# Optimization experiments

Hardware: AMD Instinct MI355X
Metric: run time of the kernel (lower is better)

## Reference

```python
import jax, jax.numpy as jnp
import numpy as np

N_NODES = 50000
HEADS = 8
NEG_SLOPE = 0.2


def _gat_conv(x, src, dst, n, W, a_src, a_dst, b, concat):
    # W: [H*C, F_in], a_src/a_dst: [H, C], b: [H*C] or [C]
    H, C = a_src.shape
    h = (x @ W.T).reshape(-1, H, C)                      # [N, H, C]
    al_src = jnp.einsum('nhc,hc->nh', h, a_src)          # [N, H]
    al_dst = jnp.einsum('nhc,hc->nh', h, a_dst)          # [N, H]
    e = jax.nn.leaky_relu(al_src[src] + al_dst[dst], NEG_SLOPE)  # [E, H]
    # segment softmax over incoming edges of each dst node
    m = jax.lax.stop_gradient(jax.ops.segment_max(e, dst, num_segments=n))
    ee = jnp.exp(e - m[dst])
    denom = jax.ops.segment_sum(ee, dst, num_segments=n)
    alpha = ee / denom[dst]                              # [E, H]
    out = jax.ops.segment_sum(alpha[:, :, None] * h[src], dst, num_segments=n)  # [N, H, C]
    out = out.reshape(n, H * C) if concat else out.mean(axis=1)
    return out + b


def setup_inputs() -> dict:
    key = jax.random.key(0)
    ks = jax.random.split(key, 12)
    N, F_in, Hd, H, Ncls = N_NODES, 128, 32, HEADS, 40
    E = 800000
    x = jax.random.normal(ks[0], (N, F_in), dtype=jnp.float32)
    edge_index = jax.random.randint(ks[1], (2, E), 0, N, dtype=jnp.int64)
    s1 = 1.0 / np.sqrt(F_in)
    W1 = jax.random.normal(ks[2], (H * Hd, F_in), dtype=jnp.float32) * s1
    a_src1 = jax.random.normal(ks[3], (H, Hd), dtype=jnp.float32) * 0.1
    a_dst1 = jax.random.normal(ks[4], (H, Hd), dtype=jnp.float32) * 0.1
    b1 = jnp.zeros((H * Hd,), dtype=jnp.float32)
    s2 = 1.0 / np.sqrt(H * Hd)
    W2 = jax.random.normal(ks[5], (H * Ncls, H * Hd), dtype=jnp.float32) * s2
    a_src2 = jax.random.normal(ks[6], (H, Ncls), dtype=jnp.float32) * 0.1
    a_dst2 = jax.random.normal(ks[7], (H, Ncls), dtype=jnp.float32) * 0.1
    b2 = jnp.zeros((Ncls,), dtype=jnp.float32)
    return {"x": x, "edge_index": edge_index,
            "W1": W1, "a_src1": a_src1, "a_dst1": a_dst1, "b1": b1,
            "W2": W2, "a_src2": a_src2, "a_dst2": a_dst2, "b2": b2}


def reference(x, edge_index, W1, a_src1, a_dst1, b1, W2, a_src2, a_dst2, b2):
    n = x.shape[0]
    # PyG GATConv default: add self loops
    loop = jnp.arange(n, dtype=edge_index.dtype)
    src = jnp.concatenate([edge_index[0], loop])
    dst = jnp.concatenate([edge_index[1], loop])
    # layer 1 (concat heads) -> ELU; dropout identity in eval mode
    h = _gat_conv(x, src, dst, n, W1, a_src1, a_dst1, b1, concat=True)
    h = jax.nn.elu(h)
    # layer 2 (mean over heads)
    out = _gat_conv(h, src, dst, n, W2, a_src2, a_dst2, b2, concat=False)
    return jax.nn.log_softmax(out, axis=1)
```

## Files before the change

kernel.cpp:

```cpp
#include <hip/hip_runtime.h>
#include <hip/hip_bf16.h>
#include <math.h>

typedef unsigned short ushort_t;
typedef unsigned char uchar_t;
typedef __attribute__((ext_vector_type(8))) short short8;
typedef __attribute__((ext_vector_type(4))) float f32x4;
typedef __attribute__((ext_vector_type(2))) float f32x2;
typedef __attribute__((ext_vector_type(4))) unsigned short u16x4;

#define LOG2E 1.44269504088896f

static __device__ __forceinline__ float b2f(ushort_t u) {
    union { unsigned int i; float f; } v; v.i = ((unsigned int)u) << 16; return v.f;
}
static __device__ __forceinline__ ushort_t f2b(float f) {
    unsigned int x = __float_as_uint(f);
    unsigned int r = (x + 0x7fffu + ((x >> 16) & 1u)) >> 16;
    return (ushort_t)r;
}
static __device__ __forceinline__ uchar_t f2e4m3(float f) {
    int r = __builtin_amdgcn_cvt_pk_fp8_f32(f, f, 0, false);
    return (uchar_t)(r & 0xff);
}
static __device__ __forceinline__ float exp2fast(float x) {
    return __builtin_amdgcn_exp2f(x);
}


template<int K, int Cd>
static __device__ void wa_item(const float* __restrict__ W, const float* __restrict__ as,
                               const float* __restrict__ ad, ushort_t* __restrict__ Bext,
                               int rowoff, int tid) {
    int col = tid / K, k = tid - col * K;
    const float* a = (col < 8) ? as : ad;
    int h = col & 7;
    float s = 0.f;
    #pragma unroll 4
    for (int c = 0; c < Cd; ++c)
        s += W[(size_t)(h * Cd + c) * K + k] * a[h * Cd + c];
    Bext[(size_t)(rowoff + col) * K + k] = f2b(s * LOG2E);
}

__global__ void prep_kernel(const float* __restrict__ W1, const float* __restrict__ W2,
                            const float* __restrict__ as1, const float* __restrict__ ad1,
                            const float* __restrict__ as2, const float* __restrict__ ad2,
                            ushort_t* __restrict__ w1b, ushort_t* __restrict__ w2b,
                            float* als1, float* als2, uchar_t* h1f8, uchar_t* h2f8, int n) {
    int b = blockIdx.x, t = threadIdx.x;
    if (b < 40) {
        for (int i = b * 256 + t; i < 8192 + 20480; i += 40 * 256) {
            if (i < 8192) {
                float4 v = *(const float4*)(W1 + i * 4);
                u16x4 o = { f2b(v.x), f2b(v.y), f2b(v.z), f2b(v.w) };
                *(u16x4*)(w1b + i * 4) = o;
            } else {
                int j = i - 8192;
                float4 v = *(const float4*)(W2 + j * 4);
                u16x4 o = { f2b(v.x), f2b(v.y), f2b(v.z), f2b(v.w) };
                *(u16x4*)(w2b + j * 4) = o;
            }
        }
    } else if (b < 64) {
        for (int i = (b - 40) * 256 + t; i < 2048 + 4096; i += 24 * 256) {
            if (i < 2048) wa_item<128, 32>(W1, as1, ad1, w1b, 256, i);
            else          wa_item<256, 40>(W2, as2, ad2, w2b, 320, i - 2048);
        }
    } else {
        if (t < 8) { als1[(size_t)n * 8 + t] = -1e30f; als2[(size_t)n * 8 + t] = -1e30f; }
        h1f8[(size_t)n * 256 + t] = 0;
        h2f8[(size_t)n * 320 + t] = 0;
        if (t < 64) h2f8[(size_t)n * 320 + 256 + t] = 0;
    }
}


__global__ void convx_count_kernel(const float* __restrict__ x, ushort_t* __restrict__ xb, int n4x,
                                   const int* __restrict__ ei, int E, int n, int* __restrict__ deg) {
    int b = blockIdx.x, t = threadIdx.x;
    if (b < 2048) {
        for (int i = b * 256 + t; i < n4x; i += 2048 * 256) {
            float4 v = *(const float4*)(x + i * 4);
            u16x4 o = { f2b(v.x), f2b(v.y), f2b(v.z), f2b(v.w) };
            *(u16x4*)(xb + i * 4) = o;
        }
    } else {
        int e = (b - 2048) * 256 + t;
        int Etot = E + n;
        if (e < Etot) {
            int dst = (e < E) ? ei[E + e] : (e - E);
            atomicAdd(&deg[dst], 1);
        }
    }
}


__global__ void scan_part_kernel(const int* __restrict__ deg, int* __restrict__ bsum, int n) {
    int i = blockIdx.x * 256 + threadIdx.x;
    int v = (i < n) ? ((deg[i] + 7) & ~7) : 0;
    #pragma unroll
    for (int off = 1; off < 64; off <<= 1) v += __shfl_xor(v, off);
    __shared__ int ws[4];
    int wid = threadIdx.x >> 6, lane = threadIdx.x & 63;
    if (lane == 0) ws[wid] = v;
    __syncthreads();
    if (threadIdx.x == 0) bsum[blockIdx.x] = ws[0] + ws[1] + ws[2] + ws[3];
}

__global__ void scan_top_kernel(int* __restrict__ bsum, int nb) {
    int t = threadIdx.x;
    int v = (t < nb) ? bsum[t] : 0;
    int val = v;
    int lane = t & 63, wid = t >> 6;
    #pragma unroll
    for (int off = 1; off < 64; off <<= 1) {
        int nv = __shfl_up(val, off);
        if (lane >= off) val += nv;
    }
    __shared__ int ws[4];
    if (lane == 63) ws[wid] = val;
    __syncthreads();
    int pre = 0;
    for (int w = 0; w < 4; ++w) if (w < wid) pre += ws[w];
    if (t < nb) bsum[t] = pre + val - v;
}

__global__ void scan_write_kernel(const int* __restrict__ deg, const int* __restrict__ bsum,
                                  int* __restrict__ rowptr, int* __restrict__ cursor, int n) {
    int i = blockIdx.x * 256 + threadIdx.x;
    int t = threadIdx.x;
    int v = (i < n) ? ((deg[i] + 7) & ~7) : 0;
    int val = v;
    int lane = t & 63, wid = t >> 6;
    #pragma unroll
    for (int off = 1; off < 64; off <<= 1) {
        int nv = __shfl_up(val, off);
        if (lane >= off) val += nv;
    }
    __shared__ int ws[4];
    if (lane == 63) ws[wid] = val;
    __syncthreads();
    int pre = bsum[blockIdx.x];
    for (int w = 0; w < 4; ++w) if (w < wid) pre += ws[w];
    int excl = pre + val - v;
    if (i < n) { rowptr[i] = excl; cursor[i] = excl; }
    if (i == n - 1) rowptr[n] = excl + v;
}

__global__ void scatter_kernel(const int* __restrict__ ei, int E, int n,
                               int* __restrict__ cursor, int* __restrict__ ssrc) {
    int e = blockIdx.x * blockDim.x + threadIdx.x;
    int Etot = E + n;
    if (e >= Etot) return;
    int src, dst;
    if (e < E) { src = ei[e]; dst = ei[E + e]; }
    else       { src = e - E; dst = e - E; }
    int pos = atomicAdd(&cursor[dst], 1);
    ssrc[pos] = src;
}

__global__ void pad_fill_kernel(const int* __restrict__ rowptr, const int* __restrict__ cursor,
                                int* __restrict__ ssrc, int n) {
    int i = blockIdx.x * blockDim.x + threadIdx.x;
    if (i >= n) return;
    int p = cursor[i], e = rowptr[i + 1];
    for (; p < e; ++p) ssrc[p] = n;
}


template<int NFRAG, int K>
__global__ __launch_bounds__(512) void gemm_lds_al(const ushort_t* __restrict__ A,
                                                   const ushort_t* __restrict__ B,
                                                   uchar_t* __restrict__ C,
                                                   float* __restrict__ als,
                                                   float* __restrict__ ald, int M) {
    constexpr int N = NFRAG * 16;
    constexpr int NOUT = (NFRAG - 1) * 16;
    constexpr int RS = 40;
    constexpr int NK = K / 32;
    __shared__ ushort_t Bs[2][N * RS];
    const int t = threadIdx.x;
    const int w = t >> 6, l = t & 63;
    const int r0 = blockIdx.x * 128 + w * 16;
    int arow = r0 + (l & 15);
    if (arow >= M) arow = M - 1;
    const int koff = (l >> 4) * 8;
    const ushort_t* ap = A + (size_t)arow * K + koff;

    f32x4 acc[NFRAG];
    #pragma unroll
    for (int i = 0; i < NFRAG; ++i) acc[i] = (f32x4){0.f, 0.f, 0.f, 0.f};

    auto stage = [&](int buf, int k0) {
        #pragma unroll
        for (int c = t; c < N * 4; c += 512) {
            int row = c >> 2, part = (c & 3) << 3;
            *(short8*)&Bs[buf][row * RS + part] =
                *(const short8*)(B + (size_t)row * K + k0 + part);
        }
    };

    stage(0, 0);
    __syncthreads();
    #pragma unroll
    for (int kk = 0; kk < NK; ++kk) {
        int buf = kk & 1;
        if (kk + 1 < NK) stage(buf ^ 1, (kk + 1) * 32);
        short8 a = *(const short8*)(ap + kk * 32);
        #pragma unroll
        for (int nf = 0; nf < NFRAG; ++nf) {
            short8 b = *(const short8*)&Bs[buf][(nf * 16 + (l & 15)) * RS + koff];
            acc[nf] = __builtin_amdgcn_mfma_f32_16x16x32_bf16(a, b, acc[nf], 0, 0, 0);
        }
        __syncthreads();
    }

    const int crow0 = r0 + (l >> 4) * 4;
    #pragma unroll
    for (int nf = 0; nf < NFRAG - 1; ++nf) {
        #pragma unroll
        for (int j = 0; j < 4; ++j) {
            int row = crow0 + j;
            if (row < M) C[(size_t)row * NOUT + nf * 16 + (l & 15)] = f2e4m3(acc[nf][j]);
        }
    }
    {
        int col = l & 15;
        float* dstp = (col < 8) ? als : ald;
        int h = col & 7;
        #pragma unroll
        for (int j = 0; j < 4; ++j) {
            int row = crow0 + j;
            if (row < M) dstp[(size_t)row * 8 + h] = acc[NFRAG - 1][j];
        }
    }
}


__device__ __forceinline__ float lrelu(float e) { return (e > 0.f) ? e : 0.2f * e; }

__global__ void agg1_kernel(const uchar_t* __restrict__ h1, const float* __restrict__ als,
                            const float* __restrict__ aldv, const float* __restrict__ b1,
                            const int* __restrict__ rowptr, const int* __restrict__ ssrc,
                            ushort_t* __restrict__ hout, int n) {
    int node = blockIdx.x * 4 + (threadIdx.x >> 6);
    if (node >= n) return;
    int l = threadIdx.x & 63;
    int h = l >> 3;
    float ald = aldv[node * 8 + h];
    int beg = rowptr[node], end = rowptr[node + 1];
    float den = 0.f;
    f32x2 acc01 = {0.f, 0.f}, acc23 = {0.f, 0.f};
    for (int p = beg; p < end; p += 8) {
        int4 sA = *(const int4*)(ssrc + p);
        int4 sB = *(const int4*)(ssrc + p + 4);
        float w0 = exp2fast(lrelu(als[sA.x * 8 + h] + ald));
        float w1 = exp2fast(lrelu(als[sA.y * 8 + h] + ald));
        float w2 = exp2fast(lrelu(als[sA.z * 8 + h] + ald));
        float w3 = exp2fast(lrelu(als[sA.w * 8 + h] + ald));
        float w4 = exp2fast(lrelu(als[sB.x * 8 + h] + ald));
        float w5 = exp2fast(lrelu(als[sB.y * 8 + h] + ald));
        float w6 = exp2fast(lrelu(als[sB.z * 8 + h] + ald));
        float w7 = exp2fast(lrelu(als[sB.w * 8 + h] + ald));
        int g0 = *(const int*)(h1 + (size_t)sA.x * 256 + l * 4);
        int g1 = *(const int*)(h1 + (size_t)sA.y * 256 + l * 4);
        int g2 = *(const int*)(h1 + (size_t)sA.z * 256 + l * 4);
        int g3 = *(const int*)(h1 + (size_t)sA.w * 256 + l * 4);
        int g4 = *(const int*)(h1 + (size_t)sB.x * 256 + l * 4);
        int g5 = *(const int*)(h1 + (size_t)sB.y * 256 + l * 4);
        int g6 = *(const int*)(h1 + (size_t)sB.z * 256 + l * 4);
        int g7 = *(const int*)(h1 + (size_t)sB.w * 256 + l * 4);
        den += ((w0 + w1) + (w2 + w3)) + ((w4 + w5) + (w6 + w7));
        #define DQ(g, wv) { \
            f32x2 lo = __builtin_amdgcn_cvt_pk_f32_fp8(g, false); \
            f32x2 hi = __builtin_amdgcn_cvt_pk_f32_fp8(g, true);  \
            f32x2 w2v = {wv, wv}; \
            acc01 += w2v * lo; acc23 += w2v * hi; }
        DQ(g0, w0) DQ(g1, w1) DQ(g2, w2) DQ(g3, w3)
        DQ(g4, w4) DQ(g5, w5) DQ(g6, w6) DQ(g7, w7)
        #undef DQ
    }
    float inv = 1.f / den;
    float4 bv = *(const float4*)(b1 + l * 4);
    float v0 = acc01.x * inv + bv.x, v1 = acc01.y * inv + bv.y;
    float v2 = acc23.x * inv + bv.z, v3 = acc23.y * inv + bv.w;
    u16x4 o;
    o.x = f2b((v0 > 0.f) ? v0 : __expf(v0) - 1.f);
    o.y = f2b((v1 > 0.f) ? v1 : __expf(v1) - 1.f);
    o.z = f2b((v2 > 0.f) ? v2 : __expf(v2) - 1.f);
    o.w = f2b((v3 > 0.f) ? v3 : __expf(v3) - 1.f);
    *(u16x4*)(hout + (size_t)node * 256 + l * 4) = o;
}


__global__ void agg2_kernel(const uchar_t* __restrict__ h2, const float* __restrict__ als,
                            const float* __restrict__ aldv, const float* __restrict__ b2,
                            const int* __restrict__ rowptr, const int* __restrict__ ssrc,
                            float* __restrict__ out, int n) {
    int node = blockIdx.x * 4 + (threadIdx.x >> 6);
    if (node >= n) return;
    int l = threadIdx.x & 63;
    int li = (l < 40) ? l : 0;
    int hd = li / 5;
    int cg = li - hd * 5;
    float ald = aldv[node * 8 + hd];
    int beg = rowptr[node], end = rowptr[node + 1];
    const uchar_t* base = h2 + hd * 40 + cg * 8;
    float den = 0.f;
    f32x2 acc01 = {0.f, 0.f}, acc23 = {0.f, 0.f}, acc45 = {0.f, 0.f}, acc67 = {0.f, 0.f};
    for (int p = beg; p < end; p += 8) {
        int4 sA = *(const int4*)(ssrc + p);
        int4 sB = *(const int4*)(ssrc + p + 4);
        float w0 = exp2fast(lrelu(als[sA.x * 8 + hd] + ald));
        float w1 = exp2fast(lrelu(als[sA.y * 8 + hd] + ald));
        float w2 = exp2fast(lrelu(als[sA.z * 8 + hd] + ald));
        float w3 = exp2fast(lrelu(als[sA.w * 8 + hd] + ald));
        float w4 = exp2fast(lrelu(als[sB.x * 8 + hd] + ald));
        float w5 = exp2fast(lrelu(als[sB.y * 8 + hd] + ald));
        float w6 = exp2fast(lrelu(als[sB.z * 8 + hd] + ald));
        float w7 = exp2fast(lrelu(als[sB.w * 8 + hd] + ald));
        uint2 g0 = *(const uint2*)(base + (size_t)sA.x * 320);
        uint2 g1 = *(const uint2*)(base + (size_t)sA.y * 320);
        uint2 g2 = *(const uint2*)(base + (size_t)sA.z * 320);
        uint2 g3 = *(const uint2*)(base + (size_t)sA.w * 320);
        uint2 g4 = *(const uint2*)(base + (size_t)sB.x * 320);
        uint2 g5 = *(const uint2*)(base + (size_t)sB.y * 320);
        uint2 g6 = *(const uint2*)(base + (size_t)sB.z * 320);
        uint2 g7 = *(const uint2*)(base + (size_t)sB.w * 320);
        den += ((w0 + w1) + (w2 + w3)) + ((w4 + w5) + (w6 + w7));
        #define DQ(g, wv) { \
            f32x2 q0 = __builtin_amdgcn_cvt_pk_f32_fp8((int)g.x, false); \
            f32x2 q1 = __builtin_amdgcn_cvt_pk_f32_fp8((int)g.x, true);  \
            f32x2 q2 = __builtin_amdgcn_cvt_pk_f32_fp8((int)g.y, false); \
            f32x2 q3 = __builtin_amdgcn_cvt_pk_f32_fp8((int)g.y, true);  \
            f32x2 w2v = {wv, wv}; \
            acc01 += w2v * q0; acc23 += w2v * q1; \
            acc45 += w2v * q2; acc67 += w2v * q3; }
        DQ(g0, w0) DQ(g1, w1) DQ(g2, w2) DQ(g3, w3)
        DQ(g4, w4) DQ(g5, w5) DQ(g6, w6) DQ(g7, w7)
        #undef DQ
    }
    float inv = 1.f / den;
    float v[8] = {acc01.x * inv, acc01.y * inv, acc23.x * inv, acc23.y * inv,
                  acc45.x * inv, acc45.y * inv, acc67.x * inv, acc67.y * inv};
    #pragma unroll
    for (int j = 0; j < 8; ++j) {
        float s = v[j];
        s += __shfl_down(s, 20);
        s += __shfl_down(s, 10);
        s += __shfl_down(s, 5);
        v[j] = s;
    }
    if (l < 5) {
        float wv[8];
        #pragma unroll
        for (int j = 0; j < 8; ++j) wv[j] = 0.125f * v[j] + b2[l * 8 + j];
        float m8 = wv[0];
        #pragma unroll
        for (int j = 1; j < 8; ++j) m8 = fmaxf(m8, wv[j]);
        float mx = m8;
        #pragma unroll
        for (int k = 0; k < 5; ++k) mx = fmaxf(mx, __shfl(m8, k));
        float se8 = 0.f;
        #pragma unroll
        for (int j = 0; j < 8; ++j) se8 += __expf(wv[j] - mx);
        float se = 0.f;
        #pragma unroll
        for (int k = 0; k < 5; ++k) se += __shfl(se8, k);
        float lse = mx + __logf(se);
        float* op = out + (size_t)node * 40 + l * 8;
        float4 o0 = {wv[0] - lse, wv[1] - lse, wv[2] - lse, wv[3] - lse};
        float4 o1 = {wv[4] - lse, wv[5] - lse, wv[6] - lse, wv[7] - lse};
        *(float4*)op = o0;
        *(float4*)(op + 4) = o1;
    }
}


extern "C" void kernel_launch(void* const* d_in, const int* in_sizes, int n_in,
                              void* d_out, int out_size, void* d_ws, size_t ws_size,
                              hipStream_t stream) {
    const float* x      = (const float*)d_in[0];
    const int*   ei     = (const int*)d_in[1];
    const float* W1     = (const float*)d_in[2];
    const float* a_src1 = (const float*)d_in[3];
    const float* a_dst1 = (const float*)d_in[4];
    const float* b1     = (const float*)d_in[5];
    const float* W2     = (const float*)d_in[6];
    const float* a_src2 = (const float*)d_in[7];
    const float* a_dst2 = (const float*)d_in[8];
    const float* b2     = (const float*)d_in[9];
    float* out = (float*)d_out;

    const int n    = in_sizes[0] / 128;
    const int E    = in_sizes[1] / 2;
    const int Etot = E + n;
    const int EpM  = Etot + 7 * n + 16;
    const int nb   = (n + 255) / 256;

    char* w = (char*)d_ws;
    auto take = [&](size_t bytes) {
        char* p = w;
        w += (bytes + 255) & ~(size_t)255;
        return p;
    };
    int*      deg    = (int*)take((size_t)n * 4);
    int*      rowptr = (int*)take((size_t)(n + 1) * 4);
    int*      cursor = (int*)take((size_t)n * 4);
    int*      bsum   = (int*)take((size_t)(nb + 1) * 4);
    int*      ssrc   = (int*)take((size_t)EpM * 4);
    ushort_t* xb     = (ushort_t*)take((size_t)n * 128 * 2);
    ushort_t* w1b    = (ushort_t*)take((size_t)272 * 128 * 2);
    ushort_t* w2b    = (ushort_t*)take((size_t)336 * 256 * 2);
    uchar_t*  h1f8   = (uchar_t*)take((size_t)(n + 1) * 256);
    ushort_t* helu   = (ushort_t*)take((size_t)n * 256 * 2);
    uchar_t*  h2f8   = (uchar_t*)take((size_t)(n + 1) * 320);
    float*    als1   = (float*)take((size_t)(n + 1) * 8 * 4);
    float*    ald1   = (float*)take((size_t)n * 8 * 4);
    float*    als2   = (float*)take((size_t)(n + 1) * 8 * 4);
    float*    ald2   = (float*)take((size_t)n * 8 * 4);

    hipMemsetAsync(deg, 0, (size_t)n * 4, stream);

    prep_kernel<<<65, 256, 0, stream>>>(W1, W2, a_src1, a_dst1, a_src2, a_dst2,
                                        w1b, w2b, als1, als2, h1f8, h2f8, n);

    int eb = (Etot + 255) / 256;
    convx_count_kernel<<<2048 + eb, 256, 0, stream>>>(x, xb, n * 128 / 4, ei, E, n, deg);
    scan_part_kernel<<<nb, 256, 0, stream>>>(deg, bsum, n);
    scan_top_kernel<<<1, 256, 0, stream>>>(bsum, nb);
    scan_write_kernel<<<nb, 256, 0, stream>>>(deg, bsum, rowptr, cursor, n);
    scatter_kernel<<<eb, 256, 0, stream>>>(ei, E, n, cursor, ssrc);
    pad_fill_kernel<<<(n + 255) / 256, 256, 0, stream>>>(rowptr, cursor, ssrc, n);

    int gb = (n + 127) / 128;
    int nb4 = (n + 3) / 4;

    gemm_lds_al<17, 128><<<gb, 512, 0, stream>>>(xb, w1b, h1f8, als1, ald1, n);
    agg1_kernel<<<nb4, 256, 0, stream>>>(h1f8, als1, ald1, b1, rowptr, ssrc, helu, n);

    gemm_lds_al<21, 256><<<gb, 512, 0, stream>>>(helu, w2b, h2f8, als2, ald2, n);
    agg2_kernel<<<nb4, 256, 0, stream>>>(h2f8, als2, ald2, b2, rowptr, ssrc, out, n);
}
```

Before: 258.2 us.

## Fold deg memset and pad fill into existing kernels; widen agg1 gather per lane

Zeroing of the degree array moves into extra blocks of the prep kernel, replacing the memset. The pad-fill kernel is removed: scan_write now prefills each row's whole padded range of ssrc with the sentinel n, and the scatter later overwrites the real slots. agg1 now has two half-waves each take 4 of every 8 edges, with each lane gathering 8 fp8 bytes instead of 4, and the halves are combined by a cross-half shuffle. This cuts two launches and halves the per-lane load count in agg1, at the cost of writes to every slot of the padded ssrc array and a final shuffle reduction.

```diff
diff --git a/kernel.cpp b/kernel.cpp
--- a/kernel.cpp
+++ b/kernel.cpp
@@ -46,7 +46,8 @@
                             const float* __restrict__ as1, const float* __restrict__ ad1,
                             const float* __restrict__ as2, const float* __restrict__ ad2,
                             ushort_t* __restrict__ w1b, ushort_t* __restrict__ w2b,
-                            float* als1, float* als2, uchar_t* h1f8, uchar_t* h2f8, int n) {
+                            float* als1, float* als2, uchar_t* h1f8, uchar_t* h2f8,
+                            int* __restrict__ deg, int n) {
     int b = blockIdx.x, t = threadIdx.x;
     if (b < 40) {
         for (int i = b * 256 + t; i < 8192 + 20480; i += 40 * 256) {
@@ -66,11 +67,14 @@
             if (i < 2048) wa_item<128, 32>(W1, as1, ad1, w1b, 256, i);
             else          wa_item<256, 40>(W2, as2, ad2, w2b, 320, i - 2048);
         }
-    } else {
+    } else if (b == 64) {
         if (t < 8) { als1[(size_t)n * 8 + t] = -1e30f; als2[(size_t)n * 8 + t] = -1e30f; }
         h1f8[(size_t)n * 256 + t] = 0;
         h2f8[(size_t)n * 320 + t] = 0;
         if (t < 64) h2f8[(size_t)n * 320 + 256 + t] = 0;
+    } else {
+        int i = (b - 65) * 256 + t;
+        if (i < n) deg[i] = 0;
     }
 }
 
@@ -126,7 +130,8 @@
 }
 
 __global__ void scan_write_kernel(const int* __restrict__ deg, const int* __restrict__ bsum,
-                                  int* __restrict__ rowptr, int* __restrict__ cursor, int n) {
+                                  int* __restrict__ rowptr, int* __restrict__ cursor,
+                                  int* __restrict__ ssrc, int n) {
     int i = blockIdx.x * 256 + threadIdx.x;
     int t = threadIdx.x;
     int v = (i < n) ? ((deg[i] + 7) & ~7) : 0;
@@ -143,7 +148,10 @@
     int pre = bsum[blockIdx.x];
     for (int w = 0; w < 4; ++w) if (w < wid) pre += ws[w];
     int excl = pre + val - v;
-    if (i < n) { rowptr[i] = excl; cursor[i] = excl; }
+    if (i < n) {
+        rowptr[i] = excl; cursor[i] = excl;
+        for (int p = excl; p < excl + v; ++p) ssrc[p] = n;
+    }
     if (i == n - 1) rowptr[n] = excl + v;
 }
 
@@ -157,14 +165,6 @@
     else       { src = e - E; dst = e - E; }
     int pos = atomicAdd(&cursor[dst], 1);
     ssrc[pos] = src;
-}
-
-__global__ void pad_fill_kernel(const int* __restrict__ rowptr, const int* __restrict__ cursor,
-                                int* __restrict__ ssrc, int n) {
-    int i = blockIdx.x * blockDim.x + threadIdx.x;
-    if (i >= n) return;
-    int p = cursor[i], e = rowptr[i + 1];
-    for (; p < e; ++p) ssrc[p] = n;
 }
 
 
@@ -246,50 +246,60 @@
     int node = blockIdx.x * 4 + (threadIdx.x >> 6);
     if (node >= n) return;
     int l = threadIdx.x & 63;
-    int h = l >> 3;
-    float ald = aldv[node * 8 + h];
+    int half = l >> 5, ll = l & 31;
+    int hd = ll >> 2;
+    float ald = aldv[node * 8 + hd];
     int beg = rowptr[node], end = rowptr[node + 1];
     float den = 0.f;
-    f32x2 acc01 = {0.f, 0.f}, acc23 = {0.f, 0.f};
+    f32x2 a0 = {0.f, 0.f}, a1 = {0.f, 0.f}, a2 = {0.f, 0.f}, a3 = {0.f, 0.f};
+    const uchar_t* fb = h1 + ll * 8;
     for (int p = beg; p < end; p += 8) {
-        int4 sA = *(const int4*)(ssrc + p);
-        int4 sB = *(const int4*)(ssrc + p + 4);
-        float w0 = exp2fast(lrelu(als[sA.x * 8 + h] + ald));
-        float w1 = exp2fast(lrelu(als[sA.y * 8 + h] + ald));
-        float w2 = exp2fast(lrelu(als[sA.z * 8 + h] + ald));
-        float w3 = exp2fast(lrelu(als[sA.w * 8 + h] + ald));
-        float w4 = exp2fast(lrelu(als[sB.x * 8 + h] + ald));
-        float w5 = exp2fast(lrelu(als[sB.y * 8 + h] + ald));
-        float w6 = exp2fast(lrelu(als[sB.z * 8 + h] + ald));
-        float w7 = exp2fast(lrelu(als[sB.w * 8 + h] + ald));
-        int g0 = *(const int*)(h1 + (size_t)sA.x * 256 + l * 4);
-        int g1 = *(const int*)(h1 + (size_t)sA.y * 256 + l * 4);
-        int g2 = *(const int*)(h1 + (size_t)sA.z * 256 + l * 4);
-        int g3 = *(const int*)(h1 + (size_t)sA.w * 256 + l * 4);
-        int g4 = *(const int*)(h1 + (size_t)sB.x * 256 + l * 4);
-        int g5 = *(const int*)(h1 + (size_t)sB.y * 256 + l * 4);
-        int g6 = *(const int*)(h1 + (size_t)sB.z * 256 + l * 4);
-        int g7 = *(const int*)(h1 + (size_t)sB.w * 256 + l * 4);
-        den += ((w0 + w1) + (w2 + w3)) + ((w4 + w5) + (w6 + w7));
+        int4 s4 = *(const int4*)(ssrc + p + half * 4);
+        float e0 = als[s4.x * 8 + hd], e1 = als[s4.y * 8 + hd];
+        float e2 = als[s4.z * 8 + hd], e3 = als[s4.w * 8 + hd];
+        uint2 g0 = *(const uint2*)(fb + (size_t)s4.x * 256);
+        uint2 g1 = *(const uint2*)(fb + (size_t)s4.y * 256);
+        uint2 g2 = *(const uint2*)(fb + (size_t)s4.z * 256);
+        uint2 g3 = *(const uint2*)(fb + (size_t)s4.w * 256);
+        float w0 = exp2fast(lrelu(e0 + ald)), w1 = exp2fast(lrelu(e1 + ald));
+        float w2 = exp2fast(lrelu(e2 + ald)), w3 = exp2fast(lrelu(e3 + ald));
+        den += (w0 + w1) + (w2 + w3);
         #define DQ(g, wv) { \
-            f32x2 lo = __builtin_amdgcn_cvt_pk_f32_fp8(g, false); \
-            f32x2 hi = __builtin_amdgcn_cvt_pk_f32_fp8(g, true);  \
+            f32x2 q0 = __builtin_amdgcn_cvt_pk_f32_fp8((int)g.x, false); \
+            f32x2 q1 = __builtin_amdgcn_cvt_pk_f32_fp8((int)g.x, true);  \
+            f32x2 q2 = __builtin_amdgcn_cvt_pk_f32_fp8((int)g.y, false); \
+            f32x2 q3 = __builtin_amdgcn_cvt_pk_f32_fp8((int)g.y, true);  \
             f32x2 w2v = {wv, wv}; \
-            acc01 += w2v * lo; acc23 += w2v * hi; }
+            a0 += w2v * q0; a1 += w2v * q1; a2 += w2v * q2; a3 += w2v * q3; }
         DQ(g0, w0) DQ(g1, w1) DQ(g2, w2) DQ(g3, w3)
-        DQ(g4, w4) DQ(g5, w5) DQ(g6, w6) DQ(g7, w7)
         #undef DQ
     }
-    float inv = 1.f / den;
-    float4 bv = *(const float4*)(b1 + l * 4);
-    float v0 = acc01.x * inv + bv.x, v1 = acc01.y * inv + bv.y;
-    float v2 = acc23.x * inv + bv.z, v3 = acc23.y * inv + bv.w;
-    u16x4 o;
-    o.x = f2b((v0 > 0.f) ? v0 : __expf(v0) - 1.f);
-    o.y = f2b((v1 > 0.f) ? v1 : __expf(v1) - 1.f);
-    o.z = f2b((v2 > 0.f) ? v2 : __expf(v2) - 1.f);
-    o.w = f2b((v3 > 0.f) ? v3 : __expf(v3) - 1.f);
-    *(u16x4*)(hout + (size_t)node * 256 + l * 4) = o;
+    den += __shfl_xor(den, 32);
+    a0.x += __shfl_xor(a0.x, 32); a0.y += __shfl_xor(a0.y, 32);
+    a1.x += __shfl_xor(a1.x, 32); a1.y += __shfl_xor(a1.y, 32);
+    a2.x += __shfl_xor(a2.x, 32); a2.y += __shfl_xor(a2.y, 32);
+    a3.x += __shfl_xor(a3.x, 32); a3.y += __shfl_xor(a3.y, 32);
+    if (half == 0) {
+        float inv = 1.f / den;
+        float4 bv0 = *(const float4*)(b1 + ll * 8);
+        float4 bv1 = *(const float4*)(b1 + ll * 8 + 4);
+        float v0 = a0.x * inv + bv0.x, v1 = a0.y * inv + bv0.y;
+        float v2 = a1.x * inv + bv0.z, v3 = a1.y * inv + bv0.w;
+        float v4 = a2.x * inv + bv1.x, v5 = a2.y * inv + bv1.y;
+        float v6 = a3.x * inv + bv1.z, v7 = a3.y * inv + bv1.w;
+        u16x4 o0, o1;
+        o0.x = f2b((v0 > 0.f) ? v0 : __expf(v0) - 1.f);
+        o0.y = f2b((v1 > 0.f) ? v1 : __expf(v1) - 1.f);
+        o0.z = f2b((v2 > 0.f) ? v2 : __expf(v2) - 1.f);
+        o0.w = f2b((v3 > 0.f) ? v3 : __expf(v3) - 1.f);
+        o1.x = f2b((v4 > 0.f) ? v4 : __expf(v4) - 1.f);
+        o1.y = f2b((v5 > 0.f) ? v5 : __expf(v5) - 1.f);
+        o1.z = f2b((v6 > 0.f) ? v6 : __expf(v6) - 1.f);
+        o1.w = f2b((v7 > 0.f) ? v7 : __expf(v7) - 1.f);
+        ushort_t* op = hout + (size_t)node * 256 + ll * 8;
+        *(u16x4*)op = o0;
+        *(u16x4*)(op + 4) = o1;
+    }
 }
 
 
@@ -420,18 +430,15 @@
     float*    als2   = (float*)take((size_t)(n + 1) * 8 * 4);
     float*    ald2   = (float*)take((size_t)n * 8 * 4);
 
-    hipMemsetAsync(deg, 0, (size_t)n * 4, stream);
-
-    prep_kernel<<<65, 256, 0, stream>>>(W1, W2, a_src1, a_dst1, a_src2, a_dst2,
-                                        w1b, w2b, als1, als2, h1f8, h2f8, n);
+    prep_kernel<<<65 + nb, 256, 0, stream>>>(W1, W2, a_src1, a_dst1, a_src2, a_dst2,
+                                             w1b, w2b, als1, als2, h1f8, h2f8, deg, n);
 
     int eb = (Etot + 255) / 256;
     convx_count_kernel<<<2048 + eb, 256, 0, stream>>>(x, xb, n * 128 / 4, ei, E, n, deg);
     scan_part_kernel<<<nb, 256, 0, stream>>>(deg, bsum, n);
     scan_top_kernel<<<1, 256, 0, stream>>>(bsum, nb);
-    scan_write_kernel<<<nb, 256, 0, stream>>>(deg, bsum, rowptr, cursor, n);
+    scan_write_kernel<<<nb, 256, 0, stream>>>(deg, bsum, rowptr, cursor, ssrc, n);
     scatter_kernel<<<eb, 256, 0, stream>>>(ei, E, n, cursor, ssrc);
-    pad_fill_kernel<<<(n + 255) / 256, 256, 0, stream>>>(rowptr, cursor, ssrc, n);
 
     int gb = (n + 127) / 128;
     int nb4 = (n + 3) / 4;
```

Result: faster. 250.8 us (-2.8%).
